# Performance work log

Hardware: AMD Instinct MI355X
Metric: run time of the kernel (lower is better)

## Reference

```python
import jax, jax.numpy as jnp
import numpy as np

B, S, D, E = 8, 2048, 4096, 64
EXPERT_CAPACITY = 40  # seq_len / n_experts * 1.25


def setup_inputs() -> dict:
    key = jax.random.key(0)
    k1, k2 = jax.random.split(key)
    hidden_states = jax.random.normal(k1, (B, S, D), dtype=jnp.float32)
    W = jax.random.normal(k2, (D, E), dtype=jnp.float32) * (1.0 / np.sqrt(D))
    b = jnp.zeros((E,), dtype=jnp.float32)
    return {"hidden_states": hidden_states, "W": W, "b": b}


def reference(hidden_states, W, b):
    # router logits: [B, S, E] (jitter_noise == 0, router_dtype == float32)
    router_logits = jnp.einsum('bsd,de->bse', hidden_states, W) + b
    router_probs = jax.nn.softmax(router_logits, axis=-1)
    top1_probs = jnp.max(router_probs, axis=-1)                    # [B, S]
    expert_idx = jnp.argmax(router_probs, axis=-1)                 # [B, S]
    expert_indices = jax.nn.one_hot(expert_idx, E, dtype=jnp.int32)  # [B, S, E]
    # capacity masking: cumulative token priority per expert along seq dim
    token_priority = jnp.cumsum(expert_indices, axis=-2)           # [B, S, E]
    capacity_mask = token_priority <= EXPERT_CAPACITY
    expert_indices = expert_indices * capacity_mask.astype(jnp.int32)
    num_dropped = jnp.sum(jnp.sum(expert_indices, axis=-1) == 0)
    # aux load-balancing loss
    fi = jnp.sum(expert_indices, axis=-2).astype(router_probs.dtype) / S  # [B, E]
    pi = jnp.sum(router_probs, axis=-2) / S                               # [B, E]
    aux_loss = jnp.mean(E * jnp.sum(fi * pi, axis=-1))
    return (expert_indices, top1_probs, router_probs, aux_loss, num_dropped)
```

## Files before the change

### kernel.cpp

```cpp
#include <hip/hip_runtime.h>
#include <hip/hip_bf16.h>
#include <stdint.h>

#define Bb 8
#define Ss 2048
#define Dd 4096
#define Ee 64
#define CAP 40
#define M_TOK (Bb*Ss)
#define TOP1_OFF  (M_TOK*Ee)
#define PROBS_OFF (TOP1_OFF + M_TOK)
#define AUX_OFF   (PROBS_OFF + M_TOK*Ee)
#define ND_OFF    (AUX_OFF + 1)

#define W2_OFF   0u
#define PART_OFF (1u<<20)
#define CNTT_OFF (17u<<20)
#define PIT_OFF  ((17u<<20) + (64u<<10))
#define PREF_OFF ((17u<<20) + (128u<<10))
#define EID_OFF  ((17u<<20) + (192u<<10))
#define BST_OFF  ((17u<<20) + (256u<<10))

typedef __attribute__((ext_vector_type(8))) short short8;
typedef __attribute__((ext_vector_type(4))) float f32x4;

#define FENCE() do {                                                          \
    asm volatile("" ::: "memory");                                            \
    __builtin_amdgcn_sched_barrier(0);                                        \
  } while (0)

__device__ __forceinline__ void cvt8hl(const float4 a, const float4 b,
                                       short8& hi, short8& lo) {
  __hip_bfloat162 h0 = __float22bfloat162_rn(make_float2(a.x, a.y));
  __hip_bfloat162 h1 = __float22bfloat162_rn(make_float2(a.z, a.w));
  __hip_bfloat162 h2 = __float22bfloat162_rn(make_float2(b.x, b.y));
  __hip_bfloat162 h3 = __float22bfloat162_rn(make_float2(b.z, b.w));
  float2 f0 = __bfloat1622float2(h0), f1 = __bfloat1622float2(h1);
  float2 f2 = __bfloat1622float2(h2), f3 = __bfloat1622float2(h3);
  __hip_bfloat162 l0 = __float22bfloat162_rn(make_float2(a.x - f0.x, a.y - f0.y));
  __hip_bfloat162 l1 = __float22bfloat162_rn(make_float2(a.z - f1.x, a.w - f1.y));
  __hip_bfloat162 l2 = __float22bfloat162_rn(make_float2(b.x - f2.x, b.y - f2.y));
  __hip_bfloat162 l3 = __float22bfloat162_rn(make_float2(b.z - f3.x, b.w - f3.y));
  union U { __hip_bfloat162 h[4]; short8 s; };
  U uh; uh.h[0] = h0; uh.h[1] = h1; uh.h[2] = h2; uh.h[3] = h3; hi = uh.s;
  U ul; ul.h[0] = l0; ul.h[1] = l1; ul.h[2] = l2; ul.h[3] = l3; lo = ul.s;
}

__global__ __launch_bounds__(256) void k0_wsplit(const float* __restrict__ W,
                                                 char* __restrict__ w2) {
  const int id  = blockIdx.x * 256 + threadIdx.x;
  const int l   = id & 63;
  const int g   = (id >> 6) & 3;
  const int sub = (id >> 8) & 1;
  const int c   = id >> 9;
  const int e   = g * 16 + (l & 15);
  const int kb  = c * 64 + sub * 32 + (l >> 4) * 8;
  float xs[8];
#pragma unroll
  for (int j = 0; j < 8; ++j) xs[j] = W[(size_t)(kb + j) * Ee + e];
  short8 hi, lo;
  cvt8hl(make_float4(xs[0], xs[1], xs[2], xs[3]),
         make_float4(xs[4], xs[5], xs[6], xs[7]), hi, lo);
  char* base = w2 + (size_t)c * 16384 + sub * 8192 + g * 2048 + l * 16;
  *(short8*)base = hi;
  *(short8*)(base + 1024) = lo;
}

__global__ __launch_bounds__(256, 4) void k1_gemm(
    const float* __restrict__ H, const char* __restrict__ w2,
    float* __restrict__ part) {
  __shared__ char wb[2][16384];
  const int tid = threadIdx.x;
  const int wv = tid >> 6, l = tid & 63;
  const int tg = blockIdx.x >> 2, ks = blockIdx.x & 3;
  const float* hA = H + (size_t)(tg * 64 + wv * 16 + (l & 15)) * Dd
                      + ks * 1024 + (l >> 4) * 8;
  const char* wsrc = w2 + (size_t)ks * 262144 + wv * 4096 + l * 16;

  f32x4 acc[4];
#pragma unroll
  for (int g = 0; g < 4; ++g) acc[g] = (f32x4){0.f, 0.f, 0.f, 0.f};

  float4 aX0, aX1, aX2, aX3, aY0, aY1, aY2, aY3;
  short8 ah0, al0, ah1, al1;

#define GLL16(gs, ls)                                                         \
  __builtin_amdgcn_global_load_lds(                                           \
      (const __attribute__((address_space(1))) unsigned int*)(gs),            \
      (__attribute__((address_space(3))) unsigned int*)(ls), 16, 0, 0)

#define STAGE(t, bi) {                                                        \
    const char* s_ = wsrc + (size_t)(t) * 16384;                              \
    char* d_ = &wb[bi][wv * 4096];                                            \
    GLL16(s_, d_);                 GLL16(s_ + 1024, d_ + 1024);               \
    GLL16(s_ + 2048, d_ + 2048);   GLL16(s_ + 3072, d_ + 3072); }

#define LDA(r0, r1, r2, r3, t) { const float* p_ = hA + (t) * 64;             \
    r0 = *(const float4*)(p_);      r1 = *(const float4*)(p_ + 4);            \
    r2 = *(const float4*)(p_ + 32); r3 = *(const float4*)(p_ + 36); }

#define MFMA4(ac, ah, al, wh, wl) {                                           \
    ac = __builtin_amdgcn_mfma_f32_16x16x32_bf16(ah, wh, ac, 0, 0, 0);        \
    ac = __builtin_amdgcn_mfma_f32_16x16x32_bf16(ah, wl, ac, 0, 0, 0);        \
    ac = __builtin_amdgcn_mfma_f32_16x16x32_bf16(al, wh, ac, 0, 0, 0);        \
    ac = __builtin_amdgcn_mfma_f32_16x16x32_bf16(al, wl, ac, 0, 0, 0); }

#define COMPM(bi) { const char* wp_ = &wb[bi][0] + l * 16;                    \
    _Pragma("unroll")                                                         \
    for (int g = 0; g < 4; ++g) {                                             \
      const short8 wh0 = *(const short8*)(wp_ + g * 2048);                    \
      const short8 wl0 = *(const short8*)(wp_ + g * 2048 + 1024);             \
      MFMA4(acc[g], ah0, al0, wh0, wl0);                                      \
      const short8 wh1 = *(const short8*)(wp_ + 8192 + g * 2048);             \
      const short8 wl1 = *(const short8*)(wp_ + 8192 + g * 2048 + 1024);      \
      MFMA4(acc[g], ah1, al1, wh1, wl1);                                      \
    } }

  STAGE(0, 0);
  FENCE();
  LDA(aX0, aX1, aX2, aX3, 0);
  LDA(aY0, aY1, aY2, aY3, 1);
  FENCE();
  asm volatile("s_waitcnt vmcnt(8)" ::: "memory");
  __builtin_amdgcn_s_barrier();

#pragma unroll
  for (int t = 0; t < 16; ++t) {
    const int bi = t & 1;
    if (t < 15) STAGE(t + 1, bi ^ 1);
    FENCE();
    if ((t & 1) == 0) {
      cvt8hl(aX0, aX1, ah0, al0); cvt8hl(aX2, aX3, ah1, al1);
      if (t < 14) LDA(aX0, aX1, aX2, aX3, t + 2);
    } else {
      cvt8hl(aY0, aY1, ah0, al0); cvt8hl(aY2, aY3, ah1, al1);
      if (t < 14) LDA(aY0, aY1, aY2, aY3, t + 2);
    }
    FENCE();
    COMPM(bi);
    if (t < 14)       { asm volatile("s_waitcnt vmcnt(4)" ::: "memory"); }
    else if (t == 14) { asm volatile("s_waitcnt vmcnt(0)" ::: "memory"); }
    if (t < 15) __builtin_amdgcn_s_barrier();
  }

  float* pp = part + (size_t)(tg * 4 + ks) * 4096;
#pragma unroll
  for (int g = 0; g < 4; ++g)
#pragma unroll
    for (int r = 0; r < 4; ++r)
      pp[(wv * 16 + (l >> 4) * 4 + r) * 64 + g * 16 + (l & 15)] = acc[g][r];
}

__global__ __launch_bounds__(512) void k1b_softmax(
    const float* __restrict__ part, const float* __restrict__ bias,
    float* __restrict__ out, int* __restrict__ cntT, float* __restrict__ piT,
    int* __restrict__ eid_ws) {
  __shared__ int   csh[512];
  __shared__ float psh[512];
  const int tid = threadIdx.x, wv = tid >> 6, l = tid & 63;
  const int tg = blockIdx.x;
  const float* p0 = part + (size_t)tg * 16384;

  int cnt = 0; float pis = 0.f;
  const float bl_ = bias[l];
#pragma unroll
  for (int i = 0; i < 8; ++i) {
    const int t = wv * 8 + i, tok = tg * 64 + t;
    const float v = p0[t * 64 + l] + p0[4096 + t * 64 + l] +
                    p0[8192 + t * 64 + l] + p0[12288 + t * 64 + l] + bl_;
    float m = v; int mi = l;
#pragma unroll
    for (int off = 32; off >= 1; off >>= 1) {
      const float ov = __shfl_xor(m, off);
      const int   oi = __shfl_xor(mi, off);
      if (ov > m || (ov == m && oi < mi)) { m = ov; mi = oi; }
    }
    const float ex = __expf(v - m);
    float ssum = ex;
#pragma unroll
    for (int off = 32; off >= 1; off >>= 1) ssum += __shfl_xor(ssum, off);
    const float inv = 1.0f / ssum;
    const float p = ex * inv;
    out[(size_t)PROBS_OFF + (size_t)tok * Ee + l] = p;
    if (l == 0) {
      out[TOP1_OFF + tok] = inv;
      eid_ws[tok] = mi;
    }
    cnt += (mi == l) ? 1 : 0;
    pis += p;
  }
  csh[wv * 64 + l] = cnt;
  psh[wv * 64 + l] = pis;
  __syncthreads();
  if (tid < 64) {
    int ct = 0; float pp = 0.f;
#pragma unroll
    for (int w = 0; w < 8; ++w) { ct += csh[w * 64 + tid]; pp += psh[w * 64 + tid]; }
    cntT[((size_t)(tg >> 5) * 64 + tid) * 32 + (tg & 31)] = ct;
    piT [((size_t)(tg >> 5) * 64 + tid) * 32 + (tg & 31)] = pp;
  }
}

__global__ __launch_bounds__(64) void k2_scan(const int* __restrict__ cntT,
                                              const float* __restrict__ piT,
                                              int* __restrict__ prefT,
                                              float* __restrict__ bstat) {
  const int b = blockIdx.x, e = threadIdx.x;
  const int4* src = (const int4*)(cntT + ((size_t)b * 64 + e) * 32);
  int4*       dst = (int4*)(prefT + ((size_t)b * 64 + e) * 32);
  int run = 0;
#pragma unroll
  for (int t = 0; t < 8; ++t) {
    const int4 v = src[t];
    int4 o;
    o.x = run; o.y = o.x + v.x; o.z = o.y + v.y; o.w = o.z + v.z;
    run = o.w + v.w;
    dst[t] = o;
  }
  const int tot = run;
  float ps = 0.f;
  const float4* pp = (const float4*)(piT + ((size_t)b * 64 + e) * 32);
#pragma unroll
  for (int t = 0; t < 8; ++t) { const float4 v = pp[t]; ps += v.x + v.y + v.z + v.w; }
  const float fi = (float)((tot < CAP) ? tot : CAP) * (1.0f / (float)Ss);
  const float pi = ps * (1.0f / (float)Ss);
  float fp = fi * pi;
  int   dr = (tot > CAP) ? (tot - CAP) : 0;
#pragma unroll
  for (int off = 32; off >= 1; off >>= 1) {
    fp += __shfl_xor(fp, off);
    dr += __shfl_xor(dr, off);
  }
  if (e == 0) { bstat[b] = fp; bstat[8 + b] = (float)dr; }
}

__global__ __launch_bounds__(64) void k3_indices(
    const int* __restrict__ prefT, const int* __restrict__ eid_ws,
    const float* __restrict__ bstat, float* __restrict__ out) {
  __shared__ float tile[64][64];
  const int g = blockIdx.x, lane = threadIdx.x;
  const int b = g >> 5;
  const int tok = g * 64 + lane;
  const int e = eid_ws[tok];

  unsigned long long mymask = 0ull;
  for (int j = 0; j < 64; ++j) {
    const int ej = __shfl(e, j);
    const unsigned long long bal = __ballot(ej == e);
    if (j == lane) mymask = bal;
  }
  const int lrank = __popcll(mymask & ((1ull << lane) - 1ull));
  const int prefix = prefT[((size_t)b * 64 + e) * 32 + (g & 31)];
  const float keep = (prefix + lrank < CAP) ? 1.0f : 0.0f;

#pragma unroll
  for (int j = 0; j < 64; ++j) tile[j][lane] = 0.f;
  __syncthreads();
  tile[lane][e] = keep;
  __syncthreads();

  float4*       og = (float4*)(out + (size_t)g * 64 * 64);
  const float4* ts = (const float4*)&tile[0][0];
#pragma unroll
  for (int i = 0; i < 16; ++i) og[i * 64 + lane] = ts[i * 64 + lane];

  if (g == 0 && lane == 0) {
    float s = 0.f, d = 0.f;
#pragma unroll
    for (int i = 0; i < 8; ++i) { s += bstat[i]; d += bstat[8 + i]; }
    out[AUX_OFF] = (float)Ee * s / (float)Bb;
    out[ND_OFF]  = d;
  }
}

extern "C" void kernel_launch(void* const* d_in, const int* in_sizes, int n_in,
                              void* d_out, int out_size, void* d_ws, size_t ws_size,
                              hipStream_t stream) {
  const float* H    = (const float*)d_in[0];
  const float* Wm   = (const float*)d_in[1];
  const float* bias = (const float*)d_in[2];
  float* out = (float*)d_out;
  char*  w2    = (char*) d_ws + W2_OFF;
  float* part  = (float*)((char*)d_ws + PART_OFF);
  int*   cntT  = (int*)  ((char*)d_ws + CNTT_OFF);
  float* piT   = (float*)((char*)d_ws + PIT_OFF);
  int*   prefT = (int*)  ((char*)d_ws + PREF_OFF);
  int*   eid   = (int*)  ((char*)d_ws + EID_OFF);
  float* bstat = (float*)((char*)d_ws + BST_OFF);

  hipLaunchKernelGGL(k0_wsplit,   dim3(128),  dim3(256), 0, stream, Wm, w2);
  hipLaunchKernelGGL(k1_gemm,     dim3(1024), dim3(256), 0, stream, H, w2, part);
  hipLaunchKernelGGL(k1b_softmax, dim3(256),  dim3(512), 0, stream,
                     part, bias, out, cntT, piT, eid);
  hipLaunchKernelGGL(k2_scan,     dim3(8),    dim3(64),  0, stream,
                     cntT, piT, prefT, bstat);
  hipLaunchKernelGGL(k3_indices,  dim3(256),  dim3(64),  0, stream,
                     prefT, eid, bstat, out);
}
```

Before: 89.99 us.

## Fuse softmax and scan into GEMM via last-block atomic counters

Folds the softmax/top-1 kernel and the per-batch capacity scan into the split-K GEMM kernel. Each token group's fourth finishing K-split block, and then each batch's last-finishing block, is picked with agent-scope atomic counters that k0 resets. Block indices are also remapped so the four K-splits of a token group are spread across the grid. This removes two kernel launches and their gaps, at the cost of a serialized tail inside the GEMM blocks that finish last and extra shared memory per block.

```diff
diff --git a/kernel.cpp b/kernel.cpp
--- a/kernel.cpp
+++ b/kernel.cpp
@@ -20,6 +20,7 @@
 #define PREF_OFF ((17u<<20) + (128u<<10))
 #define EID_OFF  ((17u<<20) + (192u<<10))
 #define BST_OFF  ((17u<<20) + (256u<<10))
+#define FLG_OFF  ((17u<<20) + (320u<<10))
 
 typedef __attribute__((ext_vector_type(8))) short short8;
 typedef __attribute__((ext_vector_type(4))) float f32x4;
@@ -47,8 +48,10 @@
 }
 
 __global__ __launch_bounds__(256) void k0_wsplit(const float* __restrict__ W,
-                                                 char* __restrict__ w2) {
+                                                 char* __restrict__ w2,
+                                                 int* __restrict__ flags) {
   const int id  = blockIdx.x * 256 + threadIdx.x;
+  if (id < 264) flags[id] = 0;
   const int l   = id & 63;
   const int g   = (id >> 6) & 3;
   const int sub = (id >> 8) & 1;
@@ -68,11 +71,19 @@
 
 __global__ __launch_bounds__(256, 4) void k1_gemm(
     const float* __restrict__ H, const char* __restrict__ w2,
-    float* __restrict__ part) {
+    const float* __restrict__ bias, float* __restrict__ out,
+    float* __restrict__ part, int* __restrict__ cntT, float* __restrict__ piT,
+    int* __restrict__ prefT, int* __restrict__ eid_ws,
+    float* __restrict__ bstat, int* __restrict__ flags) {
   __shared__ char wb[2][16384];
+  __shared__ int   csh[256];
+  __shared__ float psh[256];
+  __shared__ int s_last1, s_last2;
   const int tid = threadIdx.x;
   const int wv = tid >> 6, l = tid & 63;
-  const int tg = blockIdx.x >> 2, ks = blockIdx.x & 3;
+  const int x = blockIdx.x & 7, q = blockIdx.x >> 3;
+  const int tg = (q >> 2) * 8 + x;
+  const int ks = q & 3;
   const float* hA = H + (size_t)(tg * 64 + wv * 16 + (l & 15)) * Dd
                       + ks * 1024 + (l >> 4) * 8;
   const char* wsrc = w2 + (size_t)ks * 262144 + wv * 4096 + l * 16;
@@ -149,23 +160,22 @@
 #pragma unroll
     for (int r = 0; r < 4; ++r)
       pp[(wv * 16 + (l >> 4) * 4 + r) * 64 + g * 16 + (l & 15)] = acc[g][r];
-}
-
-__global__ __launch_bounds__(512) void k1b_softmax(
-    const float* __restrict__ part, const float* __restrict__ bias,
-    float* __restrict__ out, int* __restrict__ cntT, float* __restrict__ piT,
-    int* __restrict__ eid_ws) {
-  __shared__ int   csh[512];
-  __shared__ float psh[512];
-  const int tid = threadIdx.x, wv = tid >> 6, l = tid & 63;
-  const int tg = blockIdx.x;
+
+  __syncthreads();
+  if (tid == 0) {
+    const int r1 = __hip_atomic_fetch_add(&flags[tg], 1, __ATOMIC_ACQ_REL,
+                                          __HIP_MEMORY_SCOPE_AGENT);
+    s_last1 = (r1 == 3);
+  }
+  __syncthreads();
+  if (!s_last1) return;
+
   const float* p0 = part + (size_t)tg * 16384;
-
   int cnt = 0; float pis = 0.f;
   const float bl_ = bias[l];
-#pragma unroll
-  for (int i = 0; i < 8; ++i) {
-    const int t = wv * 8 + i, tok = tg * 64 + t;
+#pragma unroll 4
+  for (int i = 0; i < 16; ++i) {
+    const int t = wv * 16 + i, tok = tg * 64 + t;
     const float v = p0[t * 64 + l] + p0[4096 + t * 64 + l] +
                     p0[8192 + t * 64 + l] + p0[12288 + t * 64 + l] + bl_;
     float m = v; int mi = l;
@@ -192,46 +202,50 @@
   csh[wv * 64 + l] = cnt;
   psh[wv * 64 + l] = pis;
   __syncthreads();
+  const int b = tg >> 5, cc = tg & 31;
   if (tid < 64) {
-    int ct = 0; float pp = 0.f;
-#pragma unroll
-    for (int w = 0; w < 8; ++w) { ct += csh[w * 64 + tid]; pp += psh[w * 64 + tid]; }
-    cntT[((size_t)(tg >> 5) * 64 + tid) * 32 + (tg & 31)] = ct;
-    piT [((size_t)(tg >> 5) * 64 + tid) * 32 + (tg & 31)] = pp;
-  }
-}
-
-__global__ __launch_bounds__(64) void k2_scan(const int* __restrict__ cntT,
-                                              const float* __restrict__ piT,
-                                              int* __restrict__ prefT,
-                                              float* __restrict__ bstat) {
-  const int b = blockIdx.x, e = threadIdx.x;
-  const int4* src = (const int4*)(cntT + ((size_t)b * 64 + e) * 32);
-  int4*       dst = (int4*)(prefT + ((size_t)b * 64 + e) * 32);
-  int run = 0;
-#pragma unroll
-  for (int t = 0; t < 8; ++t) {
-    const int4 v = src[t];
-    int4 o;
-    o.x = run; o.y = o.x + v.x; o.z = o.y + v.y; o.w = o.z + v.z;
-    run = o.w + v.w;
-    dst[t] = o;
-  }
-  const int tot = run;
-  float ps = 0.f;
-  const float4* pp = (const float4*)(piT + ((size_t)b * 64 + e) * 32);
-#pragma unroll
-  for (int t = 0; t < 8; ++t) { const float4 v = pp[t]; ps += v.x + v.y + v.z + v.w; }
-  const float fi = (float)((tot < CAP) ? tot : CAP) * (1.0f / (float)Ss);
-  const float pi = ps * (1.0f / (float)Ss);
-  float fp = fi * pi;
-  int   dr = (tot > CAP) ? (tot - CAP) : 0;
-#pragma unroll
-  for (int off = 32; off >= 1; off >>= 1) {
-    fp += __shfl_xor(fp, off);
-    dr += __shfl_xor(dr, off);
-  }
-  if (e == 0) { bstat[b] = fp; bstat[8 + b] = (float)dr; }
+    const int   ct = csh[tid] + csh[64 + tid] + csh[128 + tid] + csh[192 + tid];
+    const float pq = psh[tid] + psh[64 + tid] + psh[128 + tid] + psh[192 + tid];
+    cntT[((size_t)b * 64 + tid) * 32 + cc] = ct;
+    piT [((size_t)b * 64 + tid) * 32 + cc] = pq;
+  }
+  __syncthreads();
+  if (tid == 0) {
+    const int r2 = __hip_atomic_fetch_add(&flags[256 + b], 1, __ATOMIC_ACQ_REL,
+                                          __HIP_MEMORY_SCOPE_AGENT);
+    s_last2 = (r2 == 31);
+  }
+  __syncthreads();
+  if (!s_last2 || wv != 0) return;
+
+  {
+    const int4* src = (const int4*)(cntT + ((size_t)b * 64 + l) * 32);
+    int4*       dst = (int4*)(prefT + ((size_t)b * 64 + l) * 32);
+    int run = 0;
+#pragma unroll
+    for (int t = 0; t < 8; ++t) {
+      const int4 v = src[t];
+      int4 o;
+      o.x = run; o.y = o.x + v.x; o.z = o.y + v.y; o.w = o.z + v.z;
+      run = o.w + v.w;
+      dst[t] = o;
+    }
+    const int tot = run;
+    float ps = 0.f;
+    const float4* pq = (const float4*)(piT + ((size_t)b * 64 + l) * 32);
+#pragma unroll
+    for (int t = 0; t < 8; ++t) { const float4 v = pq[t]; ps += v.x + v.y + v.z + v.w; }
+    const float fi = (float)((tot < CAP) ? tot : CAP) * (1.0f / (float)Ss);
+    const float pi = ps * (1.0f / (float)Ss);
+    float fp = fi * pi;
+    int   dr = (tot > CAP) ? (tot - CAP) : 0;
+#pragma unroll
+    for (int off = 32; off >= 1; off >>= 1) {
+      fp += __shfl_xor(fp, off);
+      dr += __shfl_xor(dr, off);
+    }
+    if (l == 0) { bstat[b] = fp; bstat[8 + b] = (float)dr; }
+  }
 }
 
 __global__ __launch_bounds__(64) void k3_indices(
@@ -287,13 +301,11 @@
   int*   prefT = (int*)  ((char*)d_ws + PREF_OFF);
   int*   eid   = (int*)  ((char*)d_ws + EID_OFF);
   float* bstat = (float*)((char*)d_ws + BST_OFF);
-
-  hipLaunchKernelGGL(k0_wsplit,   dim3(128),  dim3(256), 0, stream, Wm, w2);
-  hipLaunchKernelGGL(k1_gemm,     dim3(1024), dim3(256), 0, stream, H, w2, part);
-  hipLaunchKernelGGL(k1b_softmax, dim3(256),  dim3(512), 0, stream,
-                     part, bias, out, cntT, piT, eid);
-  hipLaunchKernelGGL(k2_scan,     dim3(8),    dim3(64),  0, stream,
-                     cntT, piT, prefT, bstat);
-  hipLaunchKernelGGL(k3_indices,  dim3(256),  dim3(64),  0, stream,
+  int*   flags = (int*)  ((char*)d_ws + FLG_OFF);
+
+  hipLaunchKernelGGL(k0_wsplit, dim3(128),  dim3(256), 0, stream, Wm, w2, flags);
+  hipLaunchKernelGGL(k1_gemm,   dim3(1024), dim3(256), 0, stream,
+                     H, w2, bias, out, part, cntT, piT, prefT, eid, bstat, flags);
+  hipLaunchKernelGGL(k3_indices, dim3(256), dim3(64),  0, stream,
                      prefT, eid, bstat, out);
 }
```

Result: slower. 149.7 us (+66.4%).

## Split GEMM K-dimension eight ways and fold scan kernel into index kernel

Applied to the files above, without the earlier changes.

The router GEMM now splits K into 8 slices instead of 4. This doubles the block count to 2048 and halves the per-block LDS and register footprint, targeting 8 blocks per CU for more occupancy and memory-level parallelism. The softmax kernel sums 8 partials instead of 4, which doubles partial-buffer traffic. The separate scan kernel is removed: each index block computes its own prefix from the count table, and block 0 computes the aux loss and drop count, saving one launch at the cost of some redundant small reads.

```diff
diff --git a/kernel.cpp b/kernel.cpp
--- a/kernel.cpp
+++ b/kernel.cpp
@@ -15,11 +15,9 @@
 
 #define W2_OFF   0u
 #define PART_OFF (1u<<20)
-#define CNTT_OFF (17u<<20)
-#define PIT_OFF  ((17u<<20) + (64u<<10))
-#define PREF_OFF ((17u<<20) + (128u<<10))
-#define EID_OFF  ((17u<<20) + (192u<<10))
-#define BST_OFF  ((17u<<20) + (256u<<10))
+#define CNTT_OFF (33u<<20)
+#define PIT_OFF  ((33u<<20) + (64u<<10))
+#define EID_OFF  ((33u<<20) + (128u<<10))
 
 typedef __attribute__((ext_vector_type(8))) short short8;
 typedef __attribute__((ext_vector_type(4))) float f32x4;
@@ -66,23 +64,23 @@
   *(short8*)(base + 1024) = lo;
 }
 
-__global__ __launch_bounds__(256, 4) void k1_gemm(
+__global__ __launch_bounds__(256, 8) void k1_gemm(
     const float* __restrict__ H, const char* __restrict__ w2,
     float* __restrict__ part) {
-  __shared__ char wb[2][16384];
+  __shared__ char wb[2][8192];
   const int tid = threadIdx.x;
   const int wv = tid >> 6, l = tid & 63;
-  const int tg = blockIdx.x >> 2, ks = blockIdx.x & 3;
+  const int tg = blockIdx.x >> 3, ks = blockIdx.x & 7;
   const float* hA = H + (size_t)(tg * 64 + wv * 16 + (l & 15)) * Dd
-                      + ks * 1024 + (l >> 4) * 8;
-  const char* wsrc = w2 + (size_t)ks * 262144 + wv * 4096 + l * 16;
+                      + ks * 512 + (l >> 4) * 8;
+  const char* wsrc = w2 + (size_t)ks * 131072 + wv * 2048 + l * 16;
 
   f32x4 acc[4];
 #pragma unroll
   for (int g = 0; g < 4; ++g) acc[g] = (f32x4){0.f, 0.f, 0.f, 0.f};
 
-  float4 aX0, aX1, aX2, aX3, aY0, aY1, aY2, aY3;
-  short8 ah0, al0, ah1, al1;
+  float4 aX0, aX1, aY0, aY1;
+  short8 ah0, al0;
 
 #define GLL16(gs, ls)                                                         \
   __builtin_amdgcn_global_load_lds(                                           \
@@ -90,14 +88,12 @@
       (__attribute__((address_space(3))) unsigned int*)(ls), 16, 0, 0)
 
 #define STAGE(t, bi) {                                                        \
-    const char* s_ = wsrc + (size_t)(t) * 16384;                              \
-    char* d_ = &wb[bi][wv * 4096];                                            \
-    GLL16(s_, d_);                 GLL16(s_ + 1024, d_ + 1024);               \
-    GLL16(s_ + 2048, d_ + 2048);   GLL16(s_ + 3072, d_ + 3072); }
-
-#define LDA(r0, r1, r2, r3, t) { const float* p_ = hA + (t) * 64;             \
-    r0 = *(const float4*)(p_);      r1 = *(const float4*)(p_ + 4);            \
-    r2 = *(const float4*)(p_ + 32); r3 = *(const float4*)(p_ + 36); }
+    const char* s_ = wsrc + (size_t)(t) * 8192;                               \
+    char* d_ = &wb[bi][wv * 2048];                                            \
+    GLL16(s_, d_); GLL16(s_ + 1024, d_ + 1024); }
+
+#define LDA(r0, r1, t) { const float* p_ = hA + (t) * 32;                     \
+    r0 = *(const float4*)(p_); r1 = *(const float4*)(p_ + 4); }
 
 #define MFMA4(ac, ah, al, wh, wl) {                                           \
     ac = __builtin_amdgcn_mfma_f32_16x16x32_bf16(ah, wh, ac, 0, 0, 0);        \
@@ -108,20 +104,17 @@
 #define COMPM(bi) { const char* wp_ = &wb[bi][0] + l * 16;                    \
     _Pragma("unroll")                                                         \
     for (int g = 0; g < 4; ++g) {                                             \
-      const short8 wh0 = *(const short8*)(wp_ + g * 2048);                    \
-      const short8 wl0 = *(const short8*)(wp_ + g * 2048 + 1024);             \
-      MFMA4(acc[g], ah0, al0, wh0, wl0);                                      \
-      const short8 wh1 = *(const short8*)(wp_ + 8192 + g * 2048);             \
-      const short8 wl1 = *(const short8*)(wp_ + 8192 + g * 2048 + 1024);      \
-      MFMA4(acc[g], ah1, al1, wh1, wl1);                                      \
+      const short8 wh = *(const short8*)(wp_ + g * 2048);                     \
+      const short8 wl = *(const short8*)(wp_ + g * 2048 + 1024);              \
+      MFMA4(acc[g], ah0, al0, wh, wl);                                        \
     } }
 
   STAGE(0, 0);
   FENCE();
-  LDA(aX0, aX1, aX2, aX3, 0);
-  LDA(aY0, aY1, aY2, aY3, 1);
+  LDA(aX0, aX1, 0);
+  LDA(aY0, aY1, 1);
   FENCE();
-  asm volatile("s_waitcnt vmcnt(8)" ::: "memory");
+  asm volatile("s_waitcnt vmcnt(4)" ::: "memory");
   __builtin_amdgcn_s_barrier();
 
 #pragma unroll
@@ -130,20 +123,20 @@
     if (t < 15) STAGE(t + 1, bi ^ 1);
     FENCE();
     if ((t & 1) == 0) {
-      cvt8hl(aX0, aX1, ah0, al0); cvt8hl(aX2, aX3, ah1, al1);
-      if (t < 14) LDA(aX0, aX1, aX2, aX3, t + 2);
+      cvt8hl(aX0, aX1, ah0, al0);
+      if (t < 14) LDA(aX0, aX1, t + 2);
     } else {
-      cvt8hl(aY0, aY1, ah0, al0); cvt8hl(aY2, aY3, ah1, al1);
-      if (t < 14) LDA(aY0, aY1, aY2, aY3, t + 2);
+      cvt8hl(aY0, aY1, ah0, al0);
+      if (t < 14) LDA(aY0, aY1, t + 2);
     }
     FENCE();
     COMPM(bi);
-    if (t < 14)       { asm volatile("s_waitcnt vmcnt(4)" ::: "memory"); }
+    if (t < 14)       { asm volatile("s_waitcnt vmcnt(2)" ::: "memory"); }
     else if (t == 14) { asm volatile("s_waitcnt vmcnt(0)" ::: "memory"); }
     if (t < 15) __builtin_amdgcn_s_barrier();
   }
 
-  float* pp = part + (size_t)(tg * 4 + ks) * 4096;
+  float* pp = part + (size_t)(tg * 8 + ks) * 4096;
 #pragma unroll
   for (int g = 0; g < 4; ++g)
 #pragma unroll
@@ -159,15 +152,16 @@
   __shared__ float psh[512];
   const int tid = threadIdx.x, wv = tid >> 6, l = tid & 63;
   const int tg = blockIdx.x;
-  const float* p0 = part + (size_t)tg * 16384;
+  const float* p0 = part + (size_t)tg * 32768;
 
   int cnt = 0; float pis = 0.f;
   const float bl_ = bias[l];
 #pragma unroll
   for (int i = 0; i < 8; ++i) {
     const int t = wv * 8 + i, tok = tg * 64 + t;
-    const float v = p0[t * 64 + l] + p0[4096 + t * 64 + l] +
-                    p0[8192 + t * 64 + l] + p0[12288 + t * 64 + l] + bl_;
+    float v = bl_;
+#pragma unroll
+    for (int s = 0; s < 8; ++s) v += p0[s * 4096 + t * 64 + l];
     float m = v; int mi = l;
 #pragma unroll
     for (int off = 32; off >= 1; off >>= 1) {
@@ -201,45 +195,12 @@
   }
 }
 
-__global__ __launch_bounds__(64) void k2_scan(const int* __restrict__ cntT,
-                                              const float* __restrict__ piT,
-                                              int* __restrict__ prefT,
-                                              float* __restrict__ bstat) {
-  const int b = blockIdx.x, e = threadIdx.x;
-  const int4* src = (const int4*)(cntT + ((size_t)b * 64 + e) * 32);
-  int4*       dst = (int4*)(prefT + ((size_t)b * 64 + e) * 32);
-  int run = 0;
-#pragma unroll
-  for (int t = 0; t < 8; ++t) {
-    const int4 v = src[t];
-    int4 o;
-    o.x = run; o.y = o.x + v.x; o.z = o.y + v.y; o.w = o.z + v.z;
-    run = o.w + v.w;
-    dst[t] = o;
-  }
-  const int tot = run;
-  float ps = 0.f;
-  const float4* pp = (const float4*)(piT + ((size_t)b * 64 + e) * 32);
-#pragma unroll
-  for (int t = 0; t < 8; ++t) { const float4 v = pp[t]; ps += v.x + v.y + v.z + v.w; }
-  const float fi = (float)((tot < CAP) ? tot : CAP) * (1.0f / (float)Ss);
-  const float pi = ps * (1.0f / (float)Ss);
-  float fp = fi * pi;
-  int   dr = (tot > CAP) ? (tot - CAP) : 0;
-#pragma unroll
-  for (int off = 32; off >= 1; off >>= 1) {
-    fp += __shfl_xor(fp, off);
-    dr += __shfl_xor(dr, off);
-  }
-  if (e == 0) { bstat[b] = fp; bstat[8 + b] = (float)dr; }
-}
-
 __global__ __launch_bounds__(64) void k3_indices(
-    const int* __restrict__ prefT, const int* __restrict__ eid_ws,
-    const float* __restrict__ bstat, float* __restrict__ out) {
+    const int* __restrict__ cntT, const float* __restrict__ piT,
+    const int* __restrict__ eid_ws, float* __restrict__ out) {
   __shared__ float tile[64][64];
   const int g = blockIdx.x, lane = threadIdx.x;
-  const int b = g >> 5;
+  const int b = g >> 5, cc = g & 31;
   const int tok = g * 64 + lane;
   const int e = eid_ws[tok];
 
@@ -250,7 +211,16 @@
     if (j == lane) mymask = bal;
   }
   const int lrank = __popcll(mymask & ((1ull << lane) - 1ull));
-  const int prefix = prefT[((size_t)b * 64 + e) * 32 + (g & 31)];
+
+  const int4* cp = (const int4*)(cntT + ((size_t)b * 64 + e) * 32);
+  int prefix = 0;
+#pragma unroll
+  for (int j = 0; j < 8; ++j) {
+    const int4 v = cp[j];
+    const int base = 4 * j;
+    prefix += ((base + 0 < cc) ? v.x : 0) + ((base + 1 < cc) ? v.y : 0)
+            + ((base + 2 < cc) ? v.z : 0) + ((base + 3 < cc) ? v.w : 0);
+  }
   const float keep = (prefix + lrank < CAP) ? 1.0f : 0.0f;
 
 #pragma unroll
@@ -264,12 +234,31 @@
 #pragma unroll
   for (int i = 0; i < 16; ++i) og[i * 64 + lane] = ts[i * 64 + lane];
 
-  if (g == 0 && lane == 0) {
-    float s = 0.f, d = 0.f;
-#pragma unroll
-    for (int i = 0; i < 8; ++i) { s += bstat[i]; d += bstat[8 + i]; }
-    out[AUX_OFF] = (float)Ee * s / (float)Bb;
-    out[ND_OFF]  = d;
+  if (g == 0) {
+    float auxsum = 0.f; int dropped = 0;
+    for (int bb = 0; bb < 8; ++bb) {
+      const int4*   cq = (const int4*)  (cntT + ((size_t)bb * 64 + lane) * 32);
+      const float4* pq = (const float4*)(piT  + ((size_t)bb * 64 + lane) * 32);
+      int tot = 0; float ps = 0.f;
+#pragma unroll
+      for (int j = 0; j < 8; ++j) {
+        const int4 v = cq[j];   tot += v.x + v.y + v.z + v.w;
+        const float4 w = pq[j]; ps  += w.x + w.y + w.z + w.w;
+      }
+      dropped += (tot > CAP) ? (tot - CAP) : 0;
+      const float fi = (float)((tot < CAP) ? tot : CAP) * (1.0f / (float)Ss);
+      const float pi = ps * (1.0f / (float)Ss);
+      float fp = fi * pi;
+#pragma unroll
+      for (int off = 32; off >= 1; off >>= 1) fp += __shfl_xor(fp, off);
+      auxsum += fp;
+    }
+#pragma unroll
+    for (int off = 32; off >= 1; off >>= 1) dropped += __shfl_xor(dropped, off);
+    if (lane == 0) {
+      out[AUX_OFF] = (float)Ee * auxsum / (float)Bb;
+      out[ND_OFF]  = (float)dropped;
+    }
   }
 }
 
@@ -280,20 +269,16 @@
   const float* Wm   = (const float*)d_in[1];
   const float* bias = (const float*)d_in[2];
   float* out = (float*)d_out;
-  char*  w2    = (char*) d_ws + W2_OFF;
-  float* part  = (float*)((char*)d_ws + PART_OFF);
-  int*   cntT  = (int*)  ((char*)d_ws + CNTT_OFF);
-  float* piT   = (float*)((char*)d_ws + PIT_OFF);
-  int*   prefT = (int*)  ((char*)d_ws + PREF_OFF);
-  int*   eid   = (int*)  ((char*)d_ws + EID_OFF);
-  float* bstat = (float*)((char*)d_ws + BST_OFF);
+  char*  w2   = (char*) d_ws + W2_OFF;
+  float* part = (float*)((char*)d_ws + PART_OFF);
+  int*   cntT = (int*)  ((char*)d_ws + CNTT_OFF);
+  float* piT  = (float*)((char*)d_ws + PIT_OFF);
+  int*   eid  = (int*)  ((char*)d_ws + EID_OFF);
 
   hipLaunchKernelGGL(k0_wsplit,   dim3(128),  dim3(256), 0, stream, Wm, w2);
-  hipLaunchKernelGGL(k1_gemm,     dim3(1024), dim3(256), 0, stream, H, w2, part);
+  hipLaunchKernelGGL(k1_gemm,     dim3(2048), dim3(256), 0, stream, H, w2, part);
   hipLaunchKernelGGL(k1b_softmax, dim3(256),  dim3(512), 0, stream,
                      part, bias, out, cntT, piT, eid);
-  hipLaunchKernelGGL(k2_scan,     dim3(8),    dim3(64),  0, stream,
-                     cntT, piT, prefT, bstat);
   hipLaunchKernelGGL(k3_indices,  dim3(256),  dim3(64),  0, stream,
-                     prefT, eid, bstat, out);
-}
+                     cntT, piT, eid, out);
+}
```

Measured after the change: 174.3 us. 93.7% more time.
